# Optimization experiments

Hardware: AMD Instinct MI355X
Metric: run time of the kernel (lower is better)

Reference implementation:

```python
import jax, jax.numpy as jnp
import numpy as np

N = 100000      # num nodes
E = 1600000     # num edges (avg degree 16)
IN = 128        # input_dim
D = 32          # output_dim per head
H = 4           # heads
ALPHA = 0.2     # LeakyReLU slope


def setup_inputs() -> dict:
    key = jax.random.key(0)
    k1, k2, k3, k4, k5 = jax.random.split(key, 5)
    X = jax.random.normal(k1, (N, IN), dtype=jnp.float32)
    # fc weights, xavier-like scale (bias=False in the module)
    W0 = jax.random.normal(k2, (H * D, IN), dtype=jnp.float32) * (1.0 / np.sqrt(IN))
    W1 = jax.random.normal(k3, (H * D, IN), dtype=jnp.float32) * (1.0 / np.sqrt(IN))
    a0 = jax.random.normal(k4, (H, 1, D), dtype=jnp.float32) * (1.0 / np.sqrt(D))
    deg = E // N
    # CSR rows expanded to sorted segment ids: every node has exactly `deg` out-edges
    edge_src = jnp.repeat(jnp.arange(N, dtype=jnp.int32), deg)
    column_index = jax.random.randint(k5, (E,), 0, N, dtype=jnp.int32)
    return {"X": X, "W0": W0, "W1": W1, "a0": a0,
            "edge_src": edge_src, "column_index": column_index}


def _leaky_relu(x):
    return jnp.where(x > 0, x, ALPHA * x)


def reference(X, W0, W1, a0, edge_src, column_index):
    # Linear projections, split per head: [H, N, D]
    X0 = _leaky_relu(X @ W0.T).reshape(N, H, D).transpose(1, 0, 2)
    X1 = _leaky_relu(X @ W1.T).reshape(N, H, D).transpose(1, 0, 2)
    a = a0[:, 0, :]                                    # [H, D]
    # SDDMM: att[h,e] = a[h] . (X0[h,src(e)] + X1[h,dst(e)])
    s0 = jnp.einsum('hnd,hd->hn', X0, a)               # [H, N]
    s1 = jnp.einsum('hnd,hd->hn', X1, a)
    att = s0[:, edge_src] + s1[:, column_index]        # [H, E]
    # per-head global min-max normalization, then exp (module's softmax surrogate)
    mx = jnp.max(att, axis=1, keepdims=True)
    mn = jnp.min(att, axis=1, keepdims=True)
    att = jnp.exp((att - mn) / (mx - mn))
    # sparse row-sum (softmax denominator): [N, H]
    rows_sum = jax.ops.segment_sum(att.T, edge_src, num_segments=N)
    # SpMM: aggregate neighbor features weighted by att -> [N, H, D]
    msg = att.T[:, :, None] * X1[:, column_index, :].transpose(1, 0, 2)  # [E, H, D]
    h_prime = jax.ops.segment_sum(msg, edge_src, num_segments=N)
    return h_prime / rows_sum[:, :, None]
```

## Files before the change

kernel.cpp:

```cpp
#include <hip/hip_runtime.h>
#include <hip/hip_bf16.h>
#include <stdint.h>

#define NN 100000
#define EE 1600000
#define ALPHA 0.2f
#define MM_BLOCKS 1563

typedef __bf16 bf16_t;
typedef __bf16 bf16x8 __attribute__((ext_vector_type(8)));
typedef __bf16 bf16x4 __attribute__((ext_vector_type(4)));
typedef float fx4 __attribute__((ext_vector_type(4)));


__global__ __launch_bounds__(512) void wconv_kernel(
    const float* __restrict__ W0, const float* __restrict__ W1,
    uint4* __restrict__ Wtab)
{
  const int task = blockIdx.x * 512 + threadIdx.x;
  if (task >= 4096) return;
  const int sct = task >> 8, sks = (task >> 6) & 3, sl = task & 63;
  const int r  = sct * 16 + (sl & 15);
  const int c0 = (sks * 4 + (sl >> 4)) * 8;
  const float* src = (r < 128 ? W0 + (size_t)r * 128 : W1 + (size_t)(r - 128) * 128) + c0;
  const fx4 wa = *(const fx4*)src;
  const fx4 wb = *(const fx4*)(src + 4);
  bf16x8 wf;
  wf[0] = (bf16_t)wa[0]; wf[1] = (bf16_t)wa[1];
  wf[2] = (bf16_t)wa[2]; wf[3] = (bf16_t)wa[3];
  wf[4] = (bf16_t)wb[0]; wf[5] = (bf16_t)wb[1];
  wf[6] = (bf16_t)wb[2]; wf[7] = (bf16_t)wb[3];
  Wtab[task] = __builtin_bit_cast(uint4, wf);
}

__global__ __launch_bounds__(512) void gemm_kernel(
    const float* __restrict__ X, const uint4* __restrict__ Wtab,
    const float* __restrict__ a0,
    bf16_t* __restrict__ F1, float* __restrict__ s0g, float* __restrict__ s1g)
{
  __shared__ uint4 lw[4096];
  const int tid  = threadIdx.x;
  const int wv   = tid >> 6;
  const int lane = tid & 63;
  const int col  = lane & 15;
  const int quad = lane >> 4;

#pragma unroll
  for (int i = 0; i < 8; ++i) {
    const int task = i * 512 + tid;
    __builtin_amdgcn_global_load_lds(
        (const __attribute__((address_space(1))) uint32_t*)(Wtab + task),
        (__attribute__((address_space(3))) uint32_t*)(&lw[task]), 16, 0, 0);
  }
  __syncthreads();

  const int tile = blockIdx.x * 8 + wv;
  if (tile >= (NN / 16)) return;
  const int n0   = tile * 16;
  const int node = n0 + col;

  fx4 acc[16];
#pragma unroll
  for (int c = 0; c < 16; ++c) {
    acc[c][0] = 0.f; acc[c][1] = 0.f; acc[c][2] = 0.f; acc[c][3] = 0.f;
  }

  const float* xrow = X + (size_t)node * 128 + quad * 8;
#pragma unroll
  for (int ks = 0; ks < 4; ++ks) {
    fx4 xa = *(const fx4*)(xrow + ks * 32);
    fx4 xb = *(const fx4*)(xrow + ks * 32 + 4);
    bf16x8 xf;
    xf[0] = (bf16_t)xa[0]; xf[1] = (bf16_t)xa[1];
    xf[2] = (bf16_t)xa[2]; xf[3] = (bf16_t)xa[3];
    xf[4] = (bf16_t)xb[0]; xf[5] = (bf16_t)xb[1];
    xf[6] = (bf16_t)xb[2]; xf[7] = (bf16_t)xb[3];
#pragma unroll
    for (int ct = 0; ct < 16; ++ct) {
      const uint4 w4 = lw[(ct * 4 + ks) * 64 + lane];
      const bf16x8 wf = __builtin_bit_cast(bf16x8, w4);
      acc[ct] = __builtin_amdgcn_mfma_f32_16x16x32_bf16(wf, xf, acc[ct], 0, 0, 0);
    }
  }

  float sdot[8];
#pragma unroll
  for (int s = 0; s < 8; ++s) sdot[s] = 0.f;

#pragma unroll
  for (int ct = 0; ct < 16; ++ct) {
    const fx4 av = *(const fx4*)(a0 + (ct & 7) * 16 + quad * 4);
#pragma unroll
    for (int r = 0; r < 4; ++r) {
      float v = acc[ct][r];
      v = v > 0.f ? v : ALPHA * v;
      acc[ct][r] = v;
      sdot[ct >> 1] += v * av[r];
    }
    if (ct >= 8) {
      bf16x4 p;
      p[0] = (bf16_t)acc[ct][0]; p[1] = (bf16_t)acc[ct][1];
      p[2] = (bf16_t)acc[ct][2]; p[3] = (bf16_t)acc[ct][3];
      *(bf16x4*)(F1 + (size_t)node * 128 + (ct - 8) * 16 + quad * 4) = p;
    }
  }

#pragma unroll
  for (int s = 0; s < 8; ++s) {
    sdot[s] += __shfl_xor(sdot[s], 16);
    sdot[s] += __shfl_xor(sdot[s], 32);
  }
  if (quad == 0) {
    fx4 r0, r1;
    r0[0] = sdot[0]; r0[1] = sdot[1]; r0[2] = sdot[2]; r0[3] = sdot[3];
    r1[0] = sdot[4]; r1[1] = sdot[5]; r1[2] = sdot[6]; r1[3] = sdot[7];
    *(fx4*)(s0g + (size_t)node * 4) = r0;
    *(fx4*)(s1g + (size_t)node * 4) = r1;
  }
}

__global__ __launch_bounds__(256) void minmax1_kernel(
    const int* __restrict__ cidx, const float* __restrict__ s0g,
    const float* __restrict__ s1g, float* __restrict__ partial)
{
  __shared__ float s_red[4][8];
  const int t = blockIdx.x * 256 + threadIdx.x;
  fx4 mx, mn;
#pragma unroll
  for (int h = 0; h < 4; ++h) { mx[h] = -1e30f; mn[h] = 1e30f; }
  if (t < EE / 4) {
    const int node = t >> 2;
    const fx4 s0v = *(const fx4*)(s0g + (size_t)node * 4);
    const int4 c4 = ((const int4*)cidx)[t];
    const int cc[4] = {c4.x, c4.y, c4.z, c4.w};
#pragma unroll
    for (int j = 0; j < 4; ++j) {
      const fx4 s1v = *(const fx4*)(s1g + (size_t)cc[j] * 4);
#pragma unroll
      for (int h = 0; h < 4; ++h) {
        const float att = s0v[h] + s1v[h];
        mx[h] = fmaxf(mx[h], att);
        mn[h] = fminf(mn[h], att);
      }
    }
  }
#pragma unroll
  for (int off = 1; off < 64; off <<= 1) {
#pragma unroll
    for (int h = 0; h < 4; ++h) {
      mx[h] = fmaxf(mx[h], __shfl_xor(mx[h], off));
      mn[h] = fminf(mn[h], __shfl_xor(mn[h], off));
    }
  }
  const int wv = threadIdx.x >> 6;
  if ((threadIdx.x & 63) == 0) {
#pragma unroll
    for (int h = 0; h < 4; ++h) {
      s_red[wv][h] = mx[h];
      s_red[wv][4 + h] = mn[h];
    }
  }
  __syncthreads();
  if (threadIdx.x < 8) {
    const int s = threadIdx.x;
    float v = s_red[0][s];
    if (s < 4) { v = fmaxf(v, s_red[1][s]); v = fmaxf(v, s_red[2][s]); v = fmaxf(v, s_red[3][s]); }
    else       { v = fminf(v, s_red[1][s]); v = fminf(v, s_red[2][s]); v = fminf(v, s_red[3][s]); }
    partial[blockIdx.x * 8 + s] = v;
  }
}

__global__ __launch_bounds__(256) void minmax2_kernel(
    const float* __restrict__ partial, float* __restrict__ mm)
{
  __shared__ float s_red[4][8];
  fx4 mx, mn;
#pragma unroll
  for (int h = 0; h < 4; ++h) { mx[h] = -1e30f; mn[h] = 1e30f; }
  for (int g = threadIdx.x; g < MM_BLOCKS; g += 256) {
    const fx4 p0 = *(const fx4*)(partial + g * 8);
    const fx4 p1 = *(const fx4*)(partial + g * 8 + 4);
#pragma unroll
    for (int h = 0; h < 4; ++h) {
      mx[h] = fmaxf(mx[h], p0[h]);
      mn[h] = fminf(mn[h], p1[h]);
    }
  }
#pragma unroll
  for (int off = 1; off < 64; off <<= 1) {
#pragma unroll
    for (int h = 0; h < 4; ++h) {
      mx[h] = fmaxf(mx[h], __shfl_xor(mx[h], off));
      mn[h] = fminf(mn[h], __shfl_xor(mn[h], off));
    }
  }
  const int wv = threadIdx.x >> 6;
  if ((threadIdx.x & 63) == 0) {
#pragma unroll
    for (int h = 0; h < 4; ++h) {
      s_red[wv][h] = mx[h];
      s_red[wv][4 + h] = mn[h];
    }
  }
  __syncthreads();
  if (threadIdx.x < 8) {
    const int s = threadIdx.x;
    float v = s_red[0][s];
    if (s < 4) { v = fmaxf(v, s_red[1][s]); v = fmaxf(v, s_red[2][s]); v = fmaxf(v, s_red[3][s]); }
    else       { v = fminf(v, s_red[1][s]); v = fminf(v, s_red[2][s]); v = fminf(v, s_red[3][s]); }
    mm[s] = v;
  }
}

__global__ __launch_bounds__(256) void aggregate_kernel(
    const int* __restrict__ cidx, const float* __restrict__ s0g,
    const float* __restrict__ s1g, const bf16_t* __restrict__ F1,
    const float* __restrict__ mm, float* __restrict__ out)
{
  const int t = blockIdx.x * 256 + threadIdx.x;
  const int node = t >> 4;
  if (node >= NN) return;
  const int sub = t & 15;
  const int h = sub >> 2;
  const float mxv = mm[h];
  const float mnv = mm[4 + h];
  const float scale = 1.f / (mxv - mnv);
  const float s0v = s0g[node * 4 + h];
  float a_[8] = {0.f, 0.f, 0.f, 0.f, 0.f, 0.f, 0.f, 0.f};
  float wsum = 0.f;

  const int4* ce4 = (const int4*)(cidx + (size_t)node * 16);
  const int4 c01 = ce4[0], c23 = ce4[1], c45 = ce4[2], c67 = ce4[3];
  const int cc[16] = {c01.x, c01.y, c01.z, c01.w, c23.x, c23.y, c23.z, c23.w,
                      c45.x, c45.y, c45.z, c45.w, c67.x, c67.y, c67.z, c67.w};

#pragma unroll
  for (int half = 0; half < 2; ++half) {
    float s1v[8];
    bf16x8 f[8];
#pragma unroll
    for (int j = 0; j < 8; ++j) {
      const int c = cc[half * 8 + j];
      s1v[j] = s1g[(size_t)c * 4 + h];
      f[j] = *(const bf16x8*)(F1 + (size_t)c * 128 + sub * 8);
    }
#pragma unroll
    for (int j = 0; j < 8; ++j) {
      const float w = __expf((s0v + s1v[j] - mnv) * scale);
      wsum += w;
#pragma unroll
      for (int k = 0; k < 8; ++k) a_[k] += w * (float)f[j][k];
    }
  }

  const float inv = 1.f / wsum;
  fx4 r0, r1;
#pragma unroll
  for (int j = 0; j < 4; ++j) { r0[j] = a_[j] * inv; r1[j] = a_[4 + j] * inv; }
  float* op = out + (size_t)node * 128 + sub * 8;
  *(fx4*)op = r0;
  *(fx4*)(op + 4) = r1;
}

extern "C" void kernel_launch(void* const* d_in, const int* in_sizes, int n_in,
                              void* d_out, int out_size, void* d_ws, size_t ws_size,
                              hipStream_t stream)
{
  const float* X   = (const float*)d_in[0];
  const float* W0  = (const float*)d_in[1];
  const float* W1  = (const float*)d_in[2];
  const float* a0  = (const float*)d_in[3];
  const int* cidx  = (const int*)d_in[5];
  char* ws = (char*)d_ws;
  uint4*    Wtab    = (uint4*)ws;
  bf16_t*   F1      = (bf16_t*)(ws + 65536);
  float*    s0g     = (float*)(ws + 25665536);
  float*    s1g     = (float*)(ws + 27265536);
  float*    mm      = (float*)(ws + 28865536);
  float*    partial = (float*)(ws + 28865600);
  float*    out     = (float*)d_out;

  wconv_kernel<<<8, 512, 0, stream>>>(W0, W1, Wtab);
  gemm_kernel<<<782, 512, 0, stream>>>(X, Wtab, a0, F1, s0g, s1g);
  minmax1_kernel<<<MM_BLOCKS, 256, 0, stream>>>(cidx, s0g, s1g, partial);
  minmax2_kernel<<<1, 256, 0, stream>>>(partial, mm);
  aggregate_kernel<<<6250, 256, 0, stream>>>(cidx, s0g, s1g, F1, mm, out);
}
```

Measured before the change: 207.2 us.

## Replace two-pass min-max reduction with atomics and load all 16 neighbors at once

New measurement: 226.6 us. 1.09x slower.

```diff
diff --git a/kernel.cpp b/kernel.cpp
--- a/kernel.cpp
+++ b/kernel.cpp
@@ -13,11 +13,22 @@
 typedef float fx4 __attribute__((ext_vector_type(4)));
 
 
+__device__ __forceinline__ unsigned fkey(float f) {
+  unsigned u = __float_as_uint(f);
+  return u ^ (0x80000000u | (unsigned)((int)u >> 31));
+}
+__device__ __forceinline__ float fdec(unsigned k) {
+  unsigned u = (k & 0x80000000u) ? (k ^ 0x80000000u) : ~k;
+  return __uint_as_float(u);
+}
+
 __global__ __launch_bounds__(512) void wconv_kernel(
     const float* __restrict__ W0, const float* __restrict__ W1,
-    uint4* __restrict__ Wtab)
+    uint4* __restrict__ Wtab, unsigned* __restrict__ mma)
 {
   const int task = blockIdx.x * 512 + threadIdx.x;
+  if (blockIdx.x == 0 && threadIdx.x < 8)
+    mma[threadIdx.x * 16] = (threadIdx.x < 4) ? 0u : 0xFFFFFFFFu;
   if (task >= 4096) return;
   const int sct = task >> 8, sks = (task >> 6) & 3, sl = task & 63;
   const int r  = sct * 16 + (sl & 15);
@@ -121,7 +132,7 @@
 
 __global__ __launch_bounds__(256) void minmax1_kernel(
     const int* __restrict__ cidx, const float* __restrict__ s0g,
-    const float* __restrict__ s1g, float* __restrict__ partial)
+    const float* __restrict__ s1g, unsigned* __restrict__ mma)
 {
   __shared__ float s_red[4][8];
   const int t = blockIdx.x * 256 + threadIdx.x;
@@ -164,66 +175,28 @@
   if (threadIdx.x < 8) {
     const int s = threadIdx.x;
     float v = s_red[0][s];
-    if (s < 4) { v = fmaxf(v, s_red[1][s]); v = fmaxf(v, s_red[2][s]); v = fmaxf(v, s_red[3][s]); }
-    else       { v = fminf(v, s_red[1][s]); v = fminf(v, s_red[2][s]); v = fminf(v, s_red[3][s]); }
-    partial[blockIdx.x * 8 + s] = v;
-  }
-}
-
-__global__ __launch_bounds__(256) void minmax2_kernel(
-    const float* __restrict__ partial, float* __restrict__ mm)
-{
-  __shared__ float s_red[4][8];
-  fx4 mx, mn;
-#pragma unroll
-  for (int h = 0; h < 4; ++h) { mx[h] = -1e30f; mn[h] = 1e30f; }
-  for (int g = threadIdx.x; g < MM_BLOCKS; g += 256) {
-    const fx4 p0 = *(const fx4*)(partial + g * 8);
-    const fx4 p1 = *(const fx4*)(partial + g * 8 + 4);
-#pragma unroll
-    for (int h = 0; h < 4; ++h) {
-      mx[h] = fmaxf(mx[h], p0[h]);
-      mn[h] = fminf(mn[h], p1[h]);
-    }
-  }
-#pragma unroll
-  for (int off = 1; off < 64; off <<= 1) {
-#pragma unroll
-    for (int h = 0; h < 4; ++h) {
-      mx[h] = fmaxf(mx[h], __shfl_xor(mx[h], off));
-      mn[h] = fminf(mn[h], __shfl_xor(mn[h], off));
-    }
-  }
-  const int wv = threadIdx.x >> 6;
-  if ((threadIdx.x & 63) == 0) {
-#pragma unroll
-    for (int h = 0; h < 4; ++h) {
-      s_red[wv][h] = mx[h];
-      s_red[wv][4 + h] = mn[h];
-    }
-  }
-  __syncthreads();
-  if (threadIdx.x < 8) {
-    const int s = threadIdx.x;
-    float v = s_red[0][s];
-    if (s < 4) { v = fmaxf(v, s_red[1][s]); v = fmaxf(v, s_red[2][s]); v = fmaxf(v, s_red[3][s]); }
-    else       { v = fminf(v, s_red[1][s]); v = fminf(v, s_red[2][s]); v = fminf(v, s_red[3][s]); }
-    mm[s] = v;
+    if (s < 4) {
+      v = fmaxf(v, s_red[1][s]); v = fmaxf(v, s_red[2][s]); v = fmaxf(v, s_red[3][s]);
+      atomicMax(&mma[s * 16], fkey(v));
+    } else {
+      v = fminf(v, s_red[1][s]); v = fminf(v, s_red[2][s]); v = fminf(v, s_red[3][s]);
+      atomicMin(&mma[s * 16], fkey(v));
+    }
   }
 }
 
 __global__ __launch_bounds__(256) void aggregate_kernel(
     const int* __restrict__ cidx, const float* __restrict__ s0g,
     const float* __restrict__ s1g, const bf16_t* __restrict__ F1,
-    const float* __restrict__ mm, float* __restrict__ out)
+    const unsigned* __restrict__ mma, float* __restrict__ out)
 {
   const int t = blockIdx.x * 256 + threadIdx.x;
   const int node = t >> 4;
   if (node >= NN) return;
   const int sub = t & 15;
   const int h = sub >> 2;
-  const float mxv = mm[h];
-  const float mnv = mm[4 + h];
+  const float mxv = fdec(mma[h * 16]);
+  const float mnv = fdec(mma[(4 + h) * 16]);
   const float scale = 1.f / (mxv - mnv);
   const float s0v = s0g[node * 4 + h];
   float a_[8] = {0.f, 0.f, 0.f, 0.f, 0.f, 0.f, 0.f, 0.f};
@@ -234,23 +207,22 @@
   const int cc[16] = {c01.x, c01.y, c01.z, c01.w, c23.x, c23.y, c23.z, c23.w,
                       c45.x, c45.y, c45.z, c45.w, c67.x, c67.y, c67.z, c67.w};
 
-#pragma unroll
-  for (int half = 0; half < 2; ++half) {
-    float s1v[8];
-    bf16x8 f[8];
-#pragma unroll
-    for (int j = 0; j < 8; ++j) {
-      const int c = cc[half * 8 + j];
-      s1v[j] = s1g[(size_t)c * 4 + h];
-      f[j] = *(const bf16x8*)(F1 + (size_t)c * 128 + sub * 8);
-    }
-#pragma unroll
-    for (int j = 0; j < 8; ++j) {
-      const float w = __expf((s0v + s1v[j] - mnv) * scale);
-      wsum += w;
-#pragma unroll
-      for (int k = 0; k < 8; ++k) a_[k] += w * (float)f[j][k];
-    }
+  float s1v[16];
+  bf16x8 f[16];
+#pragma unroll
+  for (int j = 0; j < 16; ++j) {
+    const int c = cc[j];
+    s1v[j] = s1g[(size_t)c * 4 + h];
+    f[j] = *(const bf16x8*)(F1 + (size_t)c * 128 + sub * 8);
+  }
+  __builtin_amdgcn_sched_barrier(0);
+
+#pragma unroll
+  for (int j = 0; j < 16; ++j) {
+    const float w = __expf((s0v + s1v[j] - mnv) * scale);
+    wsum += w;
+#pragma unroll
+    for (int k = 0; k < 8; ++k) a_[k] += w * (float)f[j][k];
   }
 
   const float inv = 1.f / wsum;
@@ -276,13 +248,11 @@
   bf16_t*   F1      = (bf16_t*)(ws + 65536);
   float*    s0g     = (float*)(ws + 25665536);
   float*    s1g     = (float*)(ws + 27265536);
-  float*    mm      = (float*)(ws + 28865536);
-  float*    partial = (float*)(ws + 28865600);
+  unsigned* mma     = (unsigned*)(ws + 28865536);
   float*    out     = (float*)d_out;
 
-  wconv_kernel<<<8, 512, 0, stream>>>(W0, W1, Wtab);
+  wconv_kernel<<<8, 512, 0, stream>>>(W0, W1, Wtab, mma);
   gemm_kernel<<<782, 512, 0, stream>>>(X, Wtab, a0, F1, s0g, s1g);
-  minmax1_kernel<<<MM_BLOCKS, 256, 0, stream>>>(cidx, s0g, s1g, partial);
-  minmax2_kernel<<<1, 256, 0, stream>>>(partial, mm);
-  aggregate_kernel<<<6250, 256, 0, stream>>>(cidx, s0g, s1g, F1, mm, out);
-}
+  minmax1_kernel<<<MM_BLOCKS, 256, 0, stream>>>(cidx, s0g, s1g, mma);
+  aggregate_kernel<<<6250, 256, 0, stream>>>(cidx, s0g, s1g, F1, mma, out);
+}
```
